# Kernel optimization log

Hardware: AMD Instinct MI355X
Metric: run time of the kernel (lower is better)

Reference implementation:

```python
import jax, jax.numpy as jnp
import numpy as np

N = 50000      # nodes
E = 800000     # edges
XS = 64        # x_size
ES = 32        # edge_attr dim (in_size = XS + ES = 96)
OUT = 64       # out_size
H = 128        # hidden_size
EPS = 1e-5


def _lin_init(k, fan_in, fan_out):
    s = 1.0 / np.sqrt(fan_in)
    kw, kb = jax.random.split(k)
    w = jax.random.uniform(kw, (fan_in, fan_out), minval=-s, maxval=s, dtype=jnp.float32)
    b = jax.random.uniform(kb, (fan_out,), minval=-s, maxval=s, dtype=jnp.float32)
    return w, b


def setup_inputs() -> dict:
    key = jax.random.key(0)
    ks = jax.random.split(key, 12)
    x = jax.random.normal(ks[0], (N, XS), dtype=jnp.float32)
    edge_index = jax.random.randint(ks[1], (2, E), 0, N, dtype=jnp.int64)
    edge_attr = jax.random.normal(ks[2], (E, ES), dtype=jnp.float32)
    u = jax.random.normal(ks[3], (1, 8), dtype=jnp.float32)
    batch = jnp.zeros((N,), dtype=jnp.int64)
    # MLP1: (96->128) LReLU (128->128) LReLU (128->64) LReLU LN(64)
    m1w0, m1b0 = _lin_init(ks[4], XS + ES, H)
    m1w1, m1b1 = _lin_init(ks[5], H, H)
    m1w2, m1b2 = _lin_init(ks[6], H, OUT)
    ln1_g = jnp.ones((OUT,), jnp.float32); ln1_b = jnp.zeros((OUT,), jnp.float32)
    # MLP2: (128->128) LReLU (128->128) LReLU (128->64) LReLU LN(64)
    m2w0, m2b0 = _lin_init(ks[7], XS + OUT, H)
    m2w1, m2b1 = _lin_init(ks[8], H, H)
    m2w2, m2b2 = _lin_init(ks[9], H, OUT)
    ln2_g = jnp.ones((OUT,), jnp.float32); ln2_b = jnp.zeros((OUT,), jnp.float32)
    return dict(x=x, edge_index=edge_index, edge_attr=edge_attr, u=u, batch=batch,
                m1w0=m1w0, m1b0=m1b0, m1w1=m1w1, m1b1=m1b1, m1w2=m1w2, m1b2=m1b2,
                ln1_g=ln1_g, ln1_b=ln1_b,
                m2w0=m2w0, m2b0=m2b0, m2w1=m2w1, m2b1=m2b1, m2w2=m2w2, m2b2=m2b2,
                ln2_g=ln2_g, ln2_b=ln2_b)


def _lrelu(v):
    return jax.nn.leaky_relu(v, 0.01)


def _layernorm(v, g, b):
    mu = jnp.mean(v, axis=-1, keepdims=True)
    var = jnp.mean(jnp.square(v - mu), axis=-1, keepdims=True)
    return (v - mu) * jax.lax.rsqrt(var + EPS) * g + b


def _mlp(h, w0, b0, w1, b1, w2, b2, g, bn):
    h = _lrelu(h @ w0 + b0)
    h = _lrelu(h @ w1 + b1)
    h = _lrelu(h @ w2 + b2)          # activate_last=True
    return _layernorm(h, g, bn)      # layer_norm=True


def reference(x, edge_index, edge_attr, u, batch,
              m1w0, m1b0, m1w1, m1b1, m1w2, m1b2, ln1_g, ln1_b,
              m2w0, m2b0, m2w1, m2b1, m2w2, m2b2, ln2_g, ln2_b):
    row, col = edge_index[0], edge_index[1]
    # gather source nodes, concat edge features -> per-edge MLP
    h = jnp.concatenate([x[row], edge_attr], axis=1)            # [E, 96]
    h = _mlp(h, m1w0, m1b0, m1w1, m1b1, m1w2, m1b2, ln1_g, ln1_b)  # [E, 64]
    # scatter_mean over destination nodes
    agg = jax.ops.segment_sum(h, col, num_segments=N)           # [N, 64]
    cnt = jax.ops.segment_sum(jnp.ones((E,), h.dtype), col, num_segments=N)
    agg = agg / jnp.maximum(cnt, 1.0)[:, None]
    # node update MLP
    h2 = jnp.concatenate([x, agg], axis=1)                      # [N, 128]
    return _mlp(h2, m2w0, m2b0, m2w1, m2b1, m2w2, m2b2, ln2_g, ln2_b)
```

## Files before the change

### kernel.cpp

```cpp
#include <hip/hip_runtime.h>


#define NNODES 50000
#define NEDGES 800000
#define NTILES_E2 3125
#define NTILES_N2 196

typedef __bf16 bf16;
typedef __bf16 __attribute__((ext_vector_type(4))) bf16x4;
typedef __bf16 __attribute__((ext_vector_type(8))) bf16x8;
typedef float __attribute__((ext_vector_type(4))) f32x4;

__device__ __forceinline__ f32x4 mfma_bf16(bf16x8 a, bf16x8 b, f32x4 c) {
    return __builtin_amdgcn_mfma_f32_16x16x32_bf16(a, b, c, 0, 0, 0);
}

__global__ void prep_weights(const float* __restrict__ w10, const float* __restrict__ w11,
                             const float* __restrict__ w12, const float* __restrict__ w20,
                             const float* __restrict__ w21, const float* __restrict__ w22,
                             bf16* __restrict__ img) {
    int idx = blockIdx.x * 256 + threadIdx.x;
    float f;
    if (idx < 13312) {
        int n = idx / 104, k = idx % 104;
        f = (k < 96) ? w10[k * 128 + n] : 0.0f;
    } else if (idx < 30720) {
        int t = idx - 13312; int n = t / 136, k = t % 136;
        f = (k < 128) ? w11[k * 128 + n] : 0.0f;
    } else if (idx < 39424) {
        int t = idx - 30720; int n = t / 136, k = t % 136;
        f = (k < 128) ? w12[k * 64 + n] : 0.0f;
    } else if (idx < 56832) {
        int t = idx - 39424; int n = t / 136, k = t % 136;
        f = (k < 128) ? w20[k * 128 + n] : 0.0f;
    } else if (idx < 74240) {
        int t = idx - 56832; int n = t / 136, k = t % 136;
        f = (k < 128) ? w21[k * 128 + n] : 0.0f;
    } else if (idx < 82944) {
        int t = idx - 74240; int n = t / 136, k = t % 136;
        f = (k < 128) ? w22[k * 64 + n] : 0.0f;
    } else {
        return;
    }
    img[idx] = (bf16)f;
}

__global__ void hist_kernel(const int* __restrict__ col, int* __restrict__ hist) {
    int i = blockIdx.x * 512 + threadIdx.x;
    if (i < NEDGES) {
        int d = col[i];
        if ((unsigned)d < (unsigned)NNODES) atomicAdd(hist + d, 1);
    }
}

__global__ void scanA(const int* __restrict__ hist, int* __restrict__ off,
                      int* __restrict__ csum) {
    __shared__ int sd[512];
    int t = threadIdx.x, i = blockIdx.x * 512 + t;
    int v = (i < NNODES) ? hist[i] : 0;
    sd[t] = v;
    __syncthreads();
    for (int o2 = 1; o2 < 512; o2 <<= 1) {
        int x = (t >= o2) ? sd[t - o2] : 0;
        __syncthreads();
        sd[t] += x;
        __syncthreads();
    }
    if (i < NNODES) off[i] = sd[t] - v;
    if (t == 511) csum[blockIdx.x] = sd[511];
}

__global__ void scanB(int* __restrict__ csum) {
    __shared__ int sd[128];
    int t = threadIdx.x;
    int v = (t < 98) ? csum[t] : 0;
    sd[t] = v;
    __syncthreads();
    for (int o2 = 1; o2 < 128; o2 <<= 1) {
        int x = (t >= o2) ? sd[t - o2] : 0;
        __syncthreads();
        sd[t] += x;
        __syncthreads();
    }
    if (t < 98) csum[t] = sd[t] - v;
}

__global__ void scanC(int* __restrict__ off, const int* __restrict__ csum) {
    int i = blockIdx.x * 512 + threadIdx.x;
    if (i < NNODES) off[i] += csum[blockIdx.x];
}

__global__ void scatter_kernel(const int* __restrict__ eidx, int* __restrict__ off,
                               int* __restrict__ perm, int* __restrict__ rdS) {
    int i = blockIdx.x * 512 + threadIdx.x;
    if (i < NEDGES) {
        int r = eidx[i], d = eidx[NEDGES + i];
        if ((unsigned)d < (unsigned)NNODES && (unsigned)r < (unsigned)NNODES) {
            int pos = atomicAdd(off + d, 1);
            if ((unsigned)pos < (unsigned)NEDGES) {
                perm[pos] = i;
                rdS[pos] = (int)(((unsigned)r & 0xFFFFu) | ((unsigned)d << 16));
            }
        }
    }
}

__global__ __launch_bounds__(512, 2) void edge_mlp(
    const float* __restrict__ x, const int* __restrict__ perm,
    const int* __restrict__ rdS, const float* __restrict__ eattr,
    const bf16* __restrict__ wimg,
    const float* __restrict__ b0g, const float* __restrict__ b1g,
    const float* __restrict__ b2g, const float* __restrict__ lng,
    const float* __restrict__ lnb, float* __restrict__ agg) {
    __shared__ __align__(16) bf16 wall[39424];
    __shared__ __align__(16) bf16 buf[256 * 136];
    __shared__ float bs[448];
    __shared__ int dstile[256];

    const int tid = threadIdx.x;
    {
        const uint4* src = (const uint4*)wimg;
        uint4* dst = (uint4*)wall;
        for (int i = tid; i < 4928; i += 512) dst[i] = src[i];
    }
    if (tid < 128) { bs[tid] = b0g[tid]; bs[128 + tid] = b1g[tid]; }
    else if (tid < 192) {
        int t = tid - 128;
        bs[256 + t] = b2g[t]; bs[320 + t] = lng[t]; bs[384 + t] = lnb[t];
    }
    __syncthreads();

    const int lane = tid & 63;
    const int wv = tid >> 6;
    const int col16 = lane & 15;
    const int quad = lane >> 4;

    float b0r[8], b1r[8], b2r[4], gr[4], br[4];
#pragma unroll
    for (int i = 0; i < 8; i++) { b0r[i] = bs[i * 16 + col16]; b1r[i] = bs[128 + i * 16 + col16]; }
#pragma unroll
    for (int i = 0; i < 4; i++) {
        b2r[i] = bs[256 + i * 16 + col16];
        gr[i] = bs[320 + i * 16 + col16];
        br[i] = bs[384 + i * 16 + col16];
    }

    const bf16* w0t = wall;
    const bf16* w1t = wall + 13312;
    const bf16* w2t = wall + 30720;

    const f32x4 vzero = {0.0f, 0.0f, 0.0f, 0.0f};
    const int r0 = wv * 32 + col16;
    const int rw = wv * 32 + quad * 4;
    const int el = tid >> 1, half = tid & 1;
    const int G = gridDim.x;

    int tile = blockIdx.x;

    float4 xr[8], er[4];
    unsigned cv;
    {
        int s = tile * 256 + el;
        cv = (unsigned)rdS[s];
        int ce = perm[s];
        int r = (int)(cv & 0xFFFFu); if (r >= NNODES) r = 0;
        if ((unsigned)ce >= (unsigned)NEDGES) ce = 0;
        const float4* xs = (const float4*)(x + (size_t)r * 64) + half * 8;
        const float4* es = (const float4*)(eattr + (size_t)ce * 32) + half * 4;
#pragma unroll
        for (int j = 0; j < 8; j++) xr[j] = xs[j];
#pragma unroll
        for (int j = 0; j < 4; j++) er[j] = es[j];
    }
    unsigned nv; int ne;
    {
        int t1 = tile + G;
        int s = (t1 < NTILES_E2 ? t1 * 256 : 0) + el;
        nv = (unsigned)rdS[s];
        ne = perm[s];
    }

    for (; tile < NTILES_E2; tile += G) {
        {
            unsigned d = cv >> 16;
            if (half == 0) dstile[el] = (d < (unsigned)NNODES) ? (int)d : 0;
            bf16* arow = buf + el * 136;
#pragma unroll
            for (int j = 0; j < 8; j++) {
                float4 vv = xr[j];
                bf16x4 u = {(bf16)vv.x, (bf16)vv.y, (bf16)vv.z, (bf16)vv.w};
                *(bf16x4*)(arow + half * 32 + j * 4) = u;
            }
#pragma unroll
            for (int j = 0; j < 4; j++) {
                float4 vv = er[j];
                bf16x4 u = {(bf16)vv.x, (bf16)vv.y, (bf16)vv.z, (bf16)vv.w};
                *(bf16x4*)(arow + 64 + half * 16 + j * 4) = u;
            }
        }
        __syncthreads();

        {
            int t2 = tile + G;
            if (t2 < NTILES_E2) {
                int r = (int)(nv & 0xFFFFu); if (r >= NNODES) r = 0;
                int e = ne; if ((unsigned)e >= (unsigned)NEDGES) e = 0;
                const float4* xs = (const float4*)(x + (size_t)r * 64) + half * 8;
                const float4* es = (const float4*)(eattr + (size_t)e * 32) + half * 4;
#pragma unroll
                for (int j = 0; j < 8; j++) xr[j] = xs[j];
#pragma unroll
                for (int j = 0; j < 4; j++) er[j] = es[j];
            }
        }
        unsigned pv; int pe;
        {
            int t3 = tile + 2 * G;
            int s = (t3 < NTILES_E2 ? t3 * 256 : 0) + el;
            pv = (unsigned)rdS[s];
            pe = perm[s];
        }

        f32x4 acc1[2][8];
#pragma unroll
        for (int mt = 0; mt < 2; mt++)
#pragma unroll
            for (int nt = 0; nt < 8; nt++) acc1[mt][nt] = vzero;
#pragma unroll
        for (int ks = 0; ks < 3; ks++) {
            bf16x8 a0 = *(const bf16x8*)(buf + r0 * 136 + ks * 32 + quad * 8);
            bf16x8 a1 = *(const bf16x8*)(buf + (r0 + 16) * 136 + ks * 32 + quad * 8);
#pragma unroll
            for (int nt = 0; nt < 8; nt++) {
                bf16x8 b = *(const bf16x8*)(w0t + (nt * 16 + col16) * 104 + ks * 32 + quad * 8);
                acc1[0][nt] = mfma_bf16(a0, b, acc1[0][nt]);
                acc1[1][nt] = mfma_bf16(a1, b, acc1[1][nt]);
            }
        }
#pragma unroll
        for (int mt = 0; mt < 2; mt++)
#pragma unroll
            for (int nt = 0; nt < 8; nt++)
#pragma unroll
                for (int rg = 0; rg < 4; rg++) {
                    float v = acc1[mt][nt][rg] + b0r[nt];
                    v = (v > 0.0f) ? v : 0.01f * v;
                    buf[(rw + mt * 16 + rg) * 136 + nt * 16 + col16] = (bf16)v;
                }

        bf16x8 a2[2][4];
#pragma unroll
        for (int mt = 0; mt < 2; mt++)
#pragma unroll
            for (int ks = 0; ks < 4; ks++)
                a2[mt][ks] = *(const bf16x8*)(buf + (r0 + mt * 16) * 136 + ks * 32 + quad * 8);
        f32x4 acc2[2][8];
#pragma unroll
        for (int mt = 0; mt < 2; mt++)
#pragma unroll
            for (int nt = 0; nt < 8; nt++) acc2[mt][nt] = vzero;
#pragma unroll
        for (int ks = 0; ks < 4; ks++) {
#pragma unroll
            for (int nt = 0; nt < 8; nt++) {
                bf16x8 b = *(const bf16x8*)(w1t + (nt * 16 + col16) * 136 + ks * 32 + quad * 8);
                acc2[0][nt] = mfma_bf16(a2[0][ks], b, acc2[0][nt]);
                acc2[1][nt] = mfma_bf16(a2[1][ks], b, acc2[1][nt]);
            }
        }
#pragma unroll
        for (int mt = 0; mt < 2; mt++)
#pragma unroll
            for (int nt = 0; nt < 8; nt++)
#pragma unroll
                for (int rg = 0; rg < 4; rg++) {
                    float v = acc2[mt][nt][rg] + b1r[nt];
                    v = (v > 0.0f) ? v : 0.01f * v;
                    buf[(rw + mt * 16 + rg) * 136 + nt * 16 + col16] = (bf16)v;
                }

        bf16x8 a3[2][4];
#pragma unroll
        for (int mt = 0; mt < 2; mt++)
#pragma unroll
            for (int ks = 0; ks < 4; ks++)
                a3[mt][ks] = *(const bf16x8*)(buf + (r0 + mt * 16) * 136 + ks * 32 + quad * 8);
        f32x4 acc3[2][4];
#pragma unroll
        for (int mt = 0; mt < 2; mt++)
#pragma unroll
            for (int nt = 0; nt < 4; nt++) acc3[mt][nt] = vzero;
#pragma unroll
        for (int ks = 0; ks < 4; ks++) {
#pragma unroll
            for (int nt = 0; nt < 4; nt++) {
                bf16x8 b = *(const bf16x8*)(w2t + (nt * 16 + col16) * 136 + ks * 32 + quad * 8);
                acc3[0][nt] = mfma_bf16(a3[0][ks], b, acc3[0][nt]);
                acc3[1][nt] = mfma_bf16(a3[1][ks], b, acc3[1][nt]);
            }
        }

        int drA[2][4];
#pragma unroll
        for (int mt = 0; mt < 2; mt++)
#pragma unroll
            for (int rg = 0; rg < 4; rg++) {
                int c = dstile[rw + mt * 16 + rg];
                drA[mt][rg] = ((unsigned)c < (unsigned)NNODES) ? c : 0;
            }
        __syncthreads();

#pragma unroll
        for (int mt = 0; mt < 2; mt++) {
            float vals[4][4];
            float s1[4] = {0.f, 0.f, 0.f, 0.f}, s2[4] = {0.f, 0.f, 0.f, 0.f};
#pragma unroll
            for (int nt = 0; nt < 4; nt++)
#pragma unroll
                for (int rg = 0; rg < 4; rg++) {
                    float v = acc3[mt][nt][rg] + b2r[nt];
                    v = (v > 0.0f) ? v : 0.01f * v;
                    vals[nt][rg] = v;
                    s1[rg] += v;
                    s2[rg] += v * v;
                }
#pragma unroll
            for (int off2 = 1; off2 < 16; off2 <<= 1) {
#pragma unroll
                for (int rg = 0; rg < 4; rg++) {
                    s1[rg] += __shfl_xor(s1[rg], off2);
                    s2[rg] += __shfl_xor(s2[rg], off2);
                }
            }
            float o[4][4];
#pragma unroll
            for (int rg = 0; rg < 4; rg++) {
                float mu = s1[rg] * 0.015625f;
                float var = s2[rg] * 0.015625f - mu * mu;
                float rstd = rsqrtf(var + 1e-5f);
#pragma unroll
                for (int nt = 0; nt < 4; nt++)
                    o[nt][rg] = (vals[nt][rg] - mu) * rstd * gr[nt] + br[nt];
            }
            float run0 = o[0][0], run1 = o[1][0], run2 = o[2][0], run3 = o[3][0];
            int cur = drA[mt][0];
#pragma unroll
            for (int rg = 1; rg < 4; rg++) {
                if (drA[mt][rg] != cur) {
                    float* dst = agg + (size_t)cur * 64 + col16;
                    atomicAdd(dst, run0); atomicAdd(dst + 16, run1);
                    atomicAdd(dst + 32, run2); atomicAdd(dst + 48, run3);
                    run0 = o[0][rg]; run1 = o[1][rg]; run2 = o[2][rg]; run3 = o[3][rg];
                    cur = drA[mt][rg];
                } else {
                    run0 += o[0][rg]; run1 += o[1][rg]; run2 += o[2][rg]; run3 += o[3][rg];
                }
            }
            float* dst = agg + (size_t)cur * 64 + col16;
            atomicAdd(dst, run0); atomicAdd(dst + 16, run1);
            atomicAdd(dst + 32, run2); atomicAdd(dst + 48, run3);
        }

        cv = nv; nv = pv; ne = pe;
    }
}

__global__ __launch_bounds__(512, 2) void node_mlp(
    const float* __restrict__ x, const float* __restrict__ agg,
    const int* __restrict__ hist, const bf16* __restrict__ wimg,
    const float* __restrict__ b0g, const float* __restrict__ b1g,
    const float* __restrict__ b2g, const float* __restrict__ lng,
    const float* __restrict__ lnb, float* __restrict__ out) {
    __shared__ __align__(16) bf16 wall[43520];
    __shared__ __align__(16) bf16 buf[256 * 136];
    __shared__ float bs[448];

    const int tid = threadIdx.x;
    {
        const uint4* src = (const uint4*)wimg;
        uint4* dst = (uint4*)wall;
        for (int i = tid; i < 5440; i += 512) dst[i] = src[i];
    }
    if (tid < 128) { bs[tid] = b0g[tid]; bs[128 + tid] = b1g[tid]; }
    else if (tid < 192) {
        int t = tid - 128;
        bs[256 + t] = b2g[t]; bs[320 + t] = lng[t]; bs[384 + t] = lnb[t];
    }
    __syncthreads();

    const int lane = tid & 63;
    const int wv = tid >> 6;
    const int col16 = lane & 15;
    const int quad = lane >> 4;

    float b0r[8], b1r[8], b2r[4], gr[4], br[4];
#pragma unroll
    for (int i = 0; i < 8; i++) { b0r[i] = bs[i * 16 + col16]; b1r[i] = bs[128 + i * 16 + col16]; }
#pragma unroll
    for (int i = 0; i < 4; i++) {
        b2r[i] = bs[256 + i * 16 + col16];
        gr[i] = bs[320 + i * 16 + col16];
        br[i] = bs[384 + i * 16 + col16];
    }

    const bf16* w0t = wall;
    const bf16* w1t = wall + 17408;
    const bf16* w2t = wall + 34816;

    const f32x4 vzero = {0.0f, 0.0f, 0.0f, 0.0f};
    const int r0 = wv * 32 + col16;
    const int rw = wv * 32 + quad * 4;
    const int el = tid >> 1, half = tid & 1;
    const int G = gridDim.x;

    int tile = blockIdx.x;
    if (tile >= NTILES_N2) return;

    float4 xr[8], ar[8];
    int cc;
    {
        int i = tile * 256 + el;
        if (i >= NNODES) i = NNODES - 1;
        const float4* xs = (const float4*)(x + (size_t)i * 64) + half * 8;
        const float4* as = (const float4*)(agg + (size_t)i * 64) + half * 8;
#pragma unroll
        for (int j = 0; j < 8; j++) { xr[j] = xs[j]; ar[j] = as[j]; }
        cc = hist[i];
    }

    for (; tile < NTILES_N2; tile += G) {
        const int nbase = tile * 256;
        {
            float inv = 1.0f / (float)(cc > 1 ? cc : 1);
            bf16* arow = buf + el * 136;
#pragma unroll
            for (int j = 0; j < 8; j++) {
                float4 v = xr[j];
                bf16x4 u = {(bf16)v.x, (bf16)v.y, (bf16)v.z, (bf16)v.w};
                *(bf16x4*)(arow + half * 32 + j * 4) = u;
            }
#pragma unroll
            for (int j = 0; j < 8; j++) {
                float4 v = ar[j];
                bf16x4 u = {(bf16)(v.x * inv), (bf16)(v.y * inv), (bf16)(v.z * inv), (bf16)(v.w * inv)};
                *(bf16x4*)(arow + 64 + half * 32 + j * 4) = u;
            }
        }
        __syncthreads();

        {
            int t2 = tile + G;
            if (t2 < NTILES_N2) {
                int i = t2 * 256 + el;
                if (i >= NNODES) i = NNODES - 1;
                const float4* xs = (const float4*)(x + (size_t)i * 64) + half * 8;
                const float4* as = (const float4*)(agg + (size_t)i * 64) + half * 8;
#pragma unroll
                for (int j = 0; j < 8; j++) { xr[j] = xs[j]; ar[j] = as[j]; }
                cc = hist[i];
            }
        }

        f32x4 acc1[2][8];
#pragma unroll
        for (int mt = 0; mt < 2; mt++)
#pragma unroll
            for (int nt = 0; nt < 8; nt++) acc1[mt][nt] = vzero;
#pragma unroll
        for (int ks = 0; ks < 4; ks++) {
            bf16x8 a0 = *(const bf16x8*)(buf + r0 * 136 + ks * 32 + quad * 8);
            bf16x8 a1 = *(const bf16x8*)(buf + (r0 + 16) * 136 + ks * 32 + quad * 8);
#pragma unroll
            for (int nt = 0; nt < 8; nt++) {
                bf16x8 b = *(const bf16x8*)(w0t + (nt * 16 + col16) * 136 + ks * 32 + quad * 8);
                acc1[0][nt] = mfma_bf16(a0, b, acc1[0][nt]);
                acc1[1][nt] = mfma_bf16(a1, b, acc1[1][nt]);
            }
        }
#pragma unroll
        for (int mt = 0; mt < 2; mt++)
#pragma unroll
            for (int nt = 0; nt < 8; nt++)
#pragma unroll
                for (int rg = 0; rg < 4; rg++) {
                    float v = acc1[mt][nt][rg] + b0r[nt];
                    v = (v > 0.0f) ? v : 0.01f * v;
                    buf[(rw + mt * 16 + rg) * 136 + nt * 16 + col16] = (bf16)v;
                }

        bf16x8 a2[2][4];
#pragma unroll
        for (int mt = 0; mt < 2; mt++)
#pragma unroll
            for (int ks = 0; ks < 4; ks++)
                a2[mt][ks] = *(const bf16x8*)(buf + (r0 + mt * 16) * 136 + ks * 32 + quad * 8);
        f32x4 acc2[2][8];
#pragma unroll
        for (int mt = 0; mt < 2; mt++)
#pragma unroll
            for (int nt = 0; nt < 8; nt++) acc2[mt][nt] = vzero;
#pragma unroll
        for (int ks = 0; ks < 4; ks++) {
#pragma unroll
            for (int nt = 0; nt < 8; nt++) {
                bf16x8 b = *(const bf16x8*)(w1t + (nt * 16 + col16) * 136 + ks * 32 + quad * 8);
                acc2[0][nt] = mfma_bf16(a2[0][ks], b, acc2[0][nt]);
                acc2[1][nt] = mfma_bf16(a2[1][ks], b, acc2[1][nt]);
            }
        }
#pragma unroll
        for (int mt = 0; mt < 2; mt++)
#pragma unroll
            for (int nt = 0; nt < 8; nt++)
#pragma unroll
                for (int rg = 0; rg < 4; rg++) {
                    float v = acc2[mt][nt][rg] + b1r[nt];
                    v = (v > 0.0f) ? v : 0.01f * v;
                    buf[(rw + mt * 16 + rg) * 136 + nt * 16 + col16] = (bf16)v;
                }

        bf16x8 a3[2][4];
#pragma unroll
        for (int mt = 0; mt < 2; mt++)
#pragma unroll
            for (int ks = 0; ks < 4; ks++)
                a3[mt][ks] = *(const bf16x8*)(buf + (r0 + mt * 16) * 136 + ks * 32 + quad * 8);
        f32x4 acc3[2][4];
#pragma unroll
        for (int mt = 0; mt < 2; mt++)
#pragma unroll
            for (int nt = 0; nt < 4; nt++) acc3[mt][nt] = vzero;
#pragma unroll
        for (int ks = 0; ks < 4; ks++) {
#pragma unroll
            for (int nt = 0; nt < 4; nt++) {
                bf16x8 b = *(const bf16x8*)(w2t + (nt * 16 + col16) * 136 + ks * 32 + quad * 8);
                acc3[0][nt] = mfma_bf16(a3[0][ks], b, acc3[0][nt]);
                acc3[1][nt] = mfma_bf16(a3[1][ks], b, acc3[1][nt]);
            }
        }
        __syncthreads();

#pragma unroll
        for (int mt = 0; mt < 2; mt++) {
            float vals[4][4];
            float s1[4] = {0.f, 0.f, 0.f, 0.f}, s2[4] = {0.f, 0.f, 0.f, 0.f};
#pragma unroll
            for (int nt = 0; nt < 4; nt++)
#pragma unroll
                for (int rg = 0; rg < 4; rg++) {
                    float v = acc3[mt][nt][rg] + b2r[nt];
                    v = (v > 0.0f) ? v : 0.01f * v;
                    vals[nt][rg] = v;
                    s1[rg] += v;
                    s2[rg] += v * v;
                }
#pragma unroll
            for (int off2 = 1; off2 < 16; off2 <<= 1) {
#pragma unroll
                for (int rg = 0; rg < 4; rg++) {
                    s1[rg] += __shfl_xor(s1[rg], off2);
                    s2[rg] += __shfl_xor(s2[rg], off2);
                }
            }
#pragma unroll
            for (int rg = 0; rg < 4; rg++) {
                float mu = s1[rg] * 0.015625f;
                float var = s2[rg] * 0.015625f - mu * mu;
                float rstd = rsqrtf(var + 1e-5f);
                int i = nbase + rw + mt * 16 + rg;
                if (i < NNODES) {
#pragma unroll
                    for (int nt = 0; nt < 4; nt++) {
                        float o = (vals[nt][rg] - mu) * rstd * gr[nt] + br[nt];
                        out[(size_t)i * 64 + nt * 16 + col16] = o;
                    }
                }
            }
        }
    }
}

extern "C" void kernel_launch(void* const* d_in, const int* in_sizes, int n_in,
                              void* d_out, int out_size, void* d_ws, size_t ws_size,
                              hipStream_t stream) {
    (void)in_sizes; (void)n_in; (void)out_size; (void)ws_size;
    const float* x     = (const float*)d_in[0];
    const int*   eidx  = (const int*)d_in[1];
    const float* eattr = (const float*)d_in[2];
    const float* m1w0 = (const float*)d_in[5];
    const float* m1b0 = (const float*)d_in[6];
    const float* m1w1 = (const float*)d_in[7];
    const float* m1b1 = (const float*)d_in[8];
    const float* m1w2 = (const float*)d_in[9];
    const float* m1b2 = (const float*)d_in[10];
    const float* ln1g = (const float*)d_in[11];
    const float* ln1b = (const float*)d_in[12];
    const float* m2w0 = (const float*)d_in[13];
    const float* m2b0 = (const float*)d_in[14];
    const float* m2w1 = (const float*)d_in[15];
    const float* m2b1 = (const float*)d_in[16];
    const float* m2w2 = (const float*)d_in[17];
    const float* m2b2 = (const float*)d_in[18];
    const float* ln2g = (const float*)d_in[19];
    const float* ln2b = (const float*)d_in[20];

    char* ws = (char*)d_ws;
    float* agg  = (float*)ws;
    int*   hist = (int*)(ws + 12800000);
    int*   off  = (int*)(ws + 13000000);
    int*   csum = (int*)(ws + 13200000);
    int*   perm = (int*)(ws + 13200512);
    int*   rdS  = (int*)(ws + 16400512);
    bf16*  wimg = (bf16*)(ws + 19600512);

    hipMemsetAsync(d_ws, 0, 13000000, stream);
    prep_weights<<<324, 256, 0, stream>>>(m1w0, m1w1, m1w2, m2w0, m2w1, m2w2, wimg);
    hist_kernel<<<1563, 512, 0, stream>>>(eidx + NEDGES, hist);
    scanA<<<98, 512, 0, stream>>>(hist, off, csum);
    scanB<<<1, 128, 0, stream>>>(csum);
    scanC<<<98, 512, 0, stream>>>(off, csum);
    scatter_kernel<<<1563, 512, 0, stream>>>(eidx, off, perm, rdS);
    edge_mlp<<<256, 512, 0, stream>>>(x, perm, rdS, eattr, wimg, m1b0, m1b1, m1b2,
                                      ln1g, ln1b, agg);
    node_mlp<<<196, 512, 0, stream>>>(x, agg, hist, wimg + 39424,
                                      m2b0, m2b1, m2b2, ln2g, ln2b, (float*)d_out);
}
```

Baseline: 489.6 us.

## Double block size to 1024 threads with one 16-row tile per wave

Both MLP kernels now run 1024-thread blocks. Each wave handles a single 16-row M tile instead of two, and four threads load each row instead of two. This halves accumulator and prefetch register pressure and puts more waves on each CU to hide gather latency. The node kernel also drops its persistent loop and prefetch, processing one tile per block. In exchange each wave reuses each loaded weight fragment for half as many MFMAs, so LDS traffic per MFMA rises.

```diff
diff --git a/kernel.cpp b/kernel.cpp
--- a/kernel.cpp
+++ b/kernel.cpp
@@ -105,7 +105,7 @@
     }
 }
 
-__global__ __launch_bounds__(512, 2) void edge_mlp(
+__global__ __launch_bounds__(1024) void edge_mlp(
     const float* __restrict__ x, const int* __restrict__ perm,
     const int* __restrict__ rdS, const float* __restrict__ eattr,
     const bf16* __restrict__ wimg,
@@ -121,7 +121,7 @@
     {
         const uint4* src = (const uint4*)wimg;
         uint4* dst = (uint4*)wall;
-        for (int i = tid; i < 4928; i += 512) dst[i] = src[i];
+        for (int i = tid; i < 4928; i += 1024) dst[i] = src[i];
     }
     if (tid < 128) { bs[tid] = b0g[tid]; bs[128 + tid] = b1g[tid]; }
     else if (tid < 192) {
@@ -150,14 +150,14 @@
     const bf16* w2t = wall + 30720;
 
     const f32x4 vzero = {0.0f, 0.0f, 0.0f, 0.0f};
-    const int r0 = wv * 32 + col16;
-    const int rw = wv * 32 + quad * 4;
-    const int el = tid >> 1, half = tid & 1;
+    const int r0 = wv * 16 + col16;
+    const int rw = wv * 16 + quad * 4;
+    const int el = tid >> 2, part = tid & 3;
     const int G = gridDim.x;
 
     int tile = blockIdx.x;
 
-    float4 xr[8], er[4];
+    float4 xr[4], er[2];
     unsigned cv;
     {
         int s = tile * 256 + el;
@@ -165,12 +165,12 @@
         int ce = perm[s];
         int r = (int)(cv & 0xFFFFu); if (r >= NNODES) r = 0;
         if ((unsigned)ce >= (unsigned)NEDGES) ce = 0;
-        const float4* xs = (const float4*)(x + (size_t)r * 64) + half * 8;
-        const float4* es = (const float4*)(eattr + (size_t)ce * 32) + half * 4;
-#pragma unroll
-        for (int j = 0; j < 8; j++) xr[j] = xs[j];
-#pragma unroll
-        for (int j = 0; j < 4; j++) er[j] = es[j];
+        const float4* xs = (const float4*)(x + (size_t)r * 64) + part * 4;
+        const float4* es = (const float4*)(eattr + (size_t)ce * 32) + part * 2;
+#pragma unroll
+        for (int j = 0; j < 4; j++) xr[j] = xs[j];
+#pragma unroll
+        for (int j = 0; j < 2; j++) er[j] = es[j];
     }
     unsigned nv; int ne;
     {
@@ -183,19 +183,19 @@
     for (; tile < NTILES_E2; tile += G) {
         {
             unsigned d = cv >> 16;
-            if (half == 0) dstile[el] = (d < (unsigned)NNODES) ? (int)d : 0;
+            if (part == 0) dstile[el] = (d < (unsigned)NNODES) ? (int)d : 0;
             bf16* arow = buf + el * 136;
 #pragma unroll
-            for (int j = 0; j < 8; j++) {
+            for (int j = 0; j < 4; j++) {
                 float4 vv = xr[j];
                 bf16x4 u = {(bf16)vv.x, (bf16)vv.y, (bf16)vv.z, (bf16)vv.w};
-                *(bf16x4*)(arow + half * 32 + j * 4) = u;
-            }
-#pragma unroll
-            for (int j = 0; j < 4; j++) {
+                *(bf16x4*)(arow + part * 16 + j * 4) = u;
+            }
+#pragma unroll
+            for (int j = 0; j < 2; j++) {
                 float4 vv = er[j];
                 bf16x4 u = {(bf16)vv.x, (bf16)vv.y, (bf16)vv.z, (bf16)vv.w};
-                *(bf16x4*)(arow + 64 + half * 16 + j * 4) = u;
+                *(bf16x4*)(arow + 64 + part * 8 + j * 4) = u;
             }
         }
         __syncthreads();
@@ -205,12 +205,12 @@
             if (t2 < NTILES_E2) {
                 int r = (int)(nv & 0xFFFFu); if (r >= NNODES) r = 0;
                 int e = ne; if ((unsigned)e >= (unsigned)NEDGES) e = 0;
-                const float4* xs = (const float4*)(x + (size_t)r * 64) + half * 8;
-                const float4* es = (const float4*)(eattr + (size_t)e * 32) + half * 4;
-#pragma unroll
-                for (int j = 0; j < 8; j++) xr[j] = xs[j];
-#pragma unroll
-                for (int j = 0; j < 4; j++) er[j] = es[j];
+                const float4* xs = (const float4*)(x + (size_t)r * 64) + part * 4;
+                const float4* es = (const float4*)(eattr + (size_t)e * 32) + part * 2;
+#pragma unroll
+                for (int j = 0; j < 4; j++) xr[j] = xs[j];
+#pragma unroll
+                for (int j = 0; j < 2; j++) er[j] = es[j];
             }
         }
         unsigned pv; int pe;
@@ -221,104 +221,83 @@
             pe = perm[s];
         }
 
-        f32x4 acc1[2][8];
-#pragma unroll
-        for (int mt = 0; mt < 2; mt++)
-#pragma unroll
-            for (int nt = 0; nt < 8; nt++) acc1[mt][nt] = vzero;
+        f32x4 acc1[8];
+#pragma unroll
+        for (int nt = 0; nt < 8; nt++) acc1[nt] = vzero;
 #pragma unroll
         for (int ks = 0; ks < 3; ks++) {
             bf16x8 a0 = *(const bf16x8*)(buf + r0 * 136 + ks * 32 + quad * 8);
-            bf16x8 a1 = *(const bf16x8*)(buf + (r0 + 16) * 136 + ks * 32 + quad * 8);
 #pragma unroll
             for (int nt = 0; nt < 8; nt++) {
                 bf16x8 b = *(const bf16x8*)(w0t + (nt * 16 + col16) * 104 + ks * 32 + quad * 8);
-                acc1[0][nt] = mfma_bf16(a0, b, acc1[0][nt]);
-                acc1[1][nt] = mfma_bf16(a1, b, acc1[1][nt]);
-            }
-        }
-#pragma unroll
-        for (int mt = 0; mt < 2; mt++)
-#pragma unroll
-            for (int nt = 0; nt < 8; nt++)
-#pragma unroll
-                for (int rg = 0; rg < 4; rg++) {
-                    float v = acc1[mt][nt][rg] + b0r[nt];
-                    v = (v > 0.0f) ? v : 0.01f * v;
-                    buf[(rw + mt * 16 + rg) * 136 + nt * 16 + col16] = (bf16)v;
-                }
-
-        bf16x8 a2[2][4];
-#pragma unroll
-        for (int mt = 0; mt < 2; mt++)
-#pragma unroll
-            for (int ks = 0; ks < 4; ks++)
-                a2[mt][ks] = *(const bf16x8*)(buf + (r0 + mt * 16) * 136 + ks * 32 + quad * 8);
-        f32x4 acc2[2][8];
-#pragma unroll
-        for (int mt = 0; mt < 2; mt++)
-#pragma unroll
-            for (int nt = 0; nt < 8; nt++) acc2[mt][nt] = vzero;
+                acc1[nt] = mfma_bf16(a0, b, acc1[nt]);
+            }
+        }
+#pragma unroll
+        for (int nt = 0; nt < 8; nt++)
+#pragma unroll
+            for (int rg = 0; rg < 4; rg++) {
+                float v = acc1[nt][rg] + b0r[nt];
+                v = (v > 0.0f) ? v : 0.01f * v;
+                buf[(rw + rg) * 136 + nt * 16 + col16] = (bf16)v;
+            }
+
+        bf16x8 a2[4];
+#pragma unroll
+        for (int ks = 0; ks < 4; ks++)
+            a2[ks] = *(const bf16x8*)(buf + r0 * 136 + ks * 32 + quad * 8);
+        f32x4 acc2[8];
+#pragma unroll
+        for (int nt = 0; nt < 8; nt++) acc2[nt] = vzero;
 #pragma unroll
         for (int ks = 0; ks < 4; ks++) {
 #pragma unroll
             for (int nt = 0; nt < 8; nt++) {
                 bf16x8 b = *(const bf16x8*)(w1t + (nt * 16 + col16) * 136 + ks * 32 + quad * 8);
-                acc2[0][nt] = mfma_bf16(a2[0][ks], b, acc2[0][nt]);
-                acc2[1][nt] = mfma_bf16(a2[1][ks], b, acc2[1][nt]);
-            }
-        }
-#pragma unroll
-        for (int mt = 0; mt < 2; mt++)
-#pragma unroll
-            for (int nt = 0; nt < 8; nt++)
-#pragma unroll
-                for (int rg = 0; rg < 4; rg++) {
-                    float v = acc2[mt][nt][rg] + b1r[nt];
-                    v = (v > 0.0f) ? v : 0.01f * v;
-                    buf[(rw + mt * 16 + rg) * 136 + nt * 16 + col16] = (bf16)v;
-                }
-
-        bf16x8 a3[2][4];
-#pragma unroll
-        for (int mt = 0; mt < 2; mt++)
-#pragma unroll
-            for (int ks = 0; ks < 4; ks++)
-                a3[mt][ks] = *(const bf16x8*)(buf + (r0 + mt * 16) * 136 + ks * 32 + quad * 8);
-        f32x4 acc3[2][4];
-#pragma unroll
-        for (int mt = 0; mt < 2; mt++)
-#pragma unroll
-            for (int nt = 0; nt < 4; nt++) acc3[mt][nt] = vzero;
+                acc2[nt] = mfma_bf16(a2[ks], b, acc2[nt]);
+            }
+        }
+#pragma unroll
+        for (int nt = 0; nt < 8; nt++)
+#pragma unroll
+            for (int rg = 0; rg < 4; rg++) {
+                float v = acc2[nt][rg] + b1r[nt];
+                v = (v > 0.0f) ? v : 0.01f * v;
+                buf[(rw + rg) * 136 + nt * 16 + col16] = (bf16)v;
+            }
+
+        bf16x8 a3[4];
+#pragma unroll
+        for (int ks = 0; ks < 4; ks++)
+            a3[ks] = *(const bf16x8*)(buf + r0 * 136 + ks * 32 + quad * 8);
+        f32x4 acc3[4];
+#pragma unroll
+        for (int nt = 0; nt < 4; nt++) acc3[nt] = vzero;
 #pragma unroll
         for (int ks = 0; ks < 4; ks++) {
 #pragma unroll
             for (int nt = 0; nt < 4; nt++) {
                 bf16x8 b = *(const bf16x8*)(w2t + (nt * 16 + col16) * 136 + ks * 32 + quad * 8);
-                acc3[0][nt] = mfma_bf16(a3[0][ks], b, acc3[0][nt]);
-                acc3[1][nt] = mfma_bf16(a3[1][ks], b, acc3[1][nt]);
-            }
-        }
-
-        int drA[2][4];
-#pragma unroll
-        for (int mt = 0; mt < 2; mt++)
-#pragma unroll
-            for (int rg = 0; rg < 4; rg++) {
-                int c = dstile[rw + mt * 16 + rg];
-                drA[mt][rg] = ((unsigned)c < (unsigned)NNODES) ? c : 0;
-            }
+                acc3[nt] = mfma_bf16(a3[ks], b, acc3[nt]);
+            }
+        }
+
+        int drA[4];
+#pragma unroll
+        for (int rg = 0; rg < 4; rg++) {
+            int c = dstile[rw + rg];
+            drA[rg] = ((unsigned)c < (unsigned)NNODES) ? c : 0;
+        }
         __syncthreads();
 
-#pragma unroll
-        for (int mt = 0; mt < 2; mt++) {
+        {
             float vals[4][4];
             float s1[4] = {0.f, 0.f, 0.f, 0.f}, s2[4] = {0.f, 0.f, 0.f, 0.f};
 #pragma unroll
             for (int nt = 0; nt < 4; nt++)
 #pragma unroll
                 for (int rg = 0; rg < 4; rg++) {
-                    float v = acc3[mt][nt][rg] + b2r[nt];
+                    float v = acc3[nt][rg] + b2r[nt];
                     v = (v > 0.0f) ? v : 0.01f * v;
                     vals[nt][rg] = v;
                     s1[rg] += v;
@@ -343,15 +322,15 @@
                     o[nt][rg] = (vals[nt][rg] - mu) * rstd * gr[nt] + br[nt];
             }
             float run0 = o[0][0], run1 = o[1][0], run2 = o[2][0], run3 = o[3][0];
-            int cur = drA[mt][0];
+            int cur = drA[0];
 #pragma unroll
             for (int rg = 1; rg < 4; rg++) {
-                if (drA[mt][rg] != cur) {
+                if (drA[rg] != cur) {
                     float* dst = agg + (size_t)cur * 64 + col16;
                     atomicAdd(dst, run0); atomicAdd(dst + 16, run1);
                     atomicAdd(dst + 32, run2); atomicAdd(dst + 48, run3);
                     run0 = o[0][rg]; run1 = o[1][rg]; run2 = o[2][rg]; run3 = o[3][rg];
-                    cur = drA[mt][rg];
+                    cur = drA[rg];
                 } else {
                     run0 += o[0][rg]; run1 += o[1][rg]; run2 += o[2][rg]; run3 += o[3][rg];
                 }
@@ -365,7 +344,7 @@
     }
 }
 
-__global__ __launch_bounds__(512, 2) void node_mlp(
+__global__ __launch_bounds__(1024) void node_mlp(
     const float* __restrict__ x, const float* __restrict__ agg,
     const int* __restrict__ hist, const bf16* __restrict__ wimg,
     const float* __restrict__ b0g, const float* __restrict__ b1g,
@@ -379,19 +358,43 @@
     {
         const uint4* src = (const uint4*)wimg;
         uint4* dst = (uint4*)wall;
-        for (int i = tid; i < 5440; i += 512) dst[i] = src[i];
+        for (int i = tid; i < 5440; i += 1024) dst[i] = src[i];
     }
     if (tid < 128) { bs[tid] = b0g[tid]; bs[128 + tid] = b1g[tid]; }
     else if (tid < 192) {
         int t = tid - 128;
         bs[256 + t] = b2g[t]; bs[320 + t] = lng[t]; bs[384 + t] = lnb[t];
     }
-    __syncthreads();
 
     const int lane = tid & 63;
     const int wv = tid >> 6;
     const int col16 = lane & 15;
     const int quad = lane >> 4;
+    const int el = tid >> 2, part = tid & 3;
+
+    const int nbase = blockIdx.x * 256;
+    {
+        int i = nbase + el;
+        if (i >= NNODES) i = NNODES - 1;
+        const float4* xs = (const float4*)(x + (size_t)i * 64) + part * 4;
+        const float4* as = (const float4*)(agg + (size_t)i * 64) + part * 4;
+        int c = hist[i];
+        float inv = 1.0f / (float)(c > 1 ? c : 1);
+        bf16* arow = buf + el * 136;
+#pragma unroll
+        for (int j = 0; j < 4; j++) {
+            float4 v = xs[j];
+            bf16x4 u = {(bf16)v.x, (bf16)v.y, (bf16)v.z, (bf16)v.w};
+            *(bf16x4*)(arow + part * 16 + j * 4) = u;
+        }
+#pragma unroll
+        for (int j = 0; j < 4; j++) {
+            float4 v = as[j];
+            bf16x4 u = {(bf16)(v.x * inv), (bf16)(v.y * inv), (bf16)(v.z * inv), (bf16)(v.w * inv)};
+            *(bf16x4*)(arow + 64 + part * 16 + j * 4) = u;
+        }
+    }
+    __syncthreads();
 
     float b0r[8], b1r[8], b2r[4], gr[4], br[4];
 #pragma unroll
@@ -408,173 +411,102 @@
     const bf16* w2t = wall + 34816;
 
     const f32x4 vzero = {0.0f, 0.0f, 0.0f, 0.0f};
-    const int r0 = wv * 32 + col16;
-    const int rw = wv * 32 + quad * 4;
-    const int el = tid >> 1, half = tid & 1;
-    const int G = gridDim.x;
-
-    int tile = blockIdx.x;
-    if (tile >= NTILES_N2) return;
-
-    float4 xr[8], ar[8];
-    int cc;
+    const int r0 = wv * 16 + col16;
+    const int rw = wv * 16 + quad * 4;
+
+    f32x4 acc1[8];
+#pragma unroll
+    for (int nt = 0; nt < 8; nt++) acc1[nt] = vzero;
+#pragma unroll
+    for (int ks = 0; ks < 4; ks++) {
+        bf16x8 a0 = *(const bf16x8*)(buf + r0 * 136 + ks * 32 + quad * 8);
+#pragma unroll
+        for (int nt = 0; nt < 8; nt++) {
+            bf16x8 b = *(const bf16x8*)(w0t + (nt * 16 + col16) * 136 + ks * 32 + quad * 8);
+            acc1[nt] = mfma_bf16(a0, b, acc1[nt]);
+        }
+    }
+#pragma unroll
+    for (int nt = 0; nt < 8; nt++)
+#pragma unroll
+        for (int rg = 0; rg < 4; rg++) {
+            float v = acc1[nt][rg] + b0r[nt];
+            v = (v > 0.0f) ? v : 0.01f * v;
+            buf[(rw + rg) * 136 + nt * 16 + col16] = (bf16)v;
+        }
+
+    bf16x8 a2[4];
+#pragma unroll
+    for (int ks = 0; ks < 4; ks++)
+        a2[ks] = *(const bf16x8*)(buf + r0 * 136 + ks * 32 + quad * 8);
+    f32x4 acc2[8];
+#pragma unroll
+    for (int nt = 0; nt < 8; nt++) acc2[nt] = vzero;
+#pragma unroll
+    for (int ks = 0; ks < 4; ks++) {
+#pragma unroll
+        for (int nt = 0; nt < 8; nt++) {
+            bf16x8 b = *(const bf16x8*)(w1t + (nt * 16 + col16) * 136 + ks * 32 + quad * 8);
+            acc2[nt] = mfma_bf16(a2[ks], b, acc2[nt]);
+        }
+    }
+#pragma unroll
+    for (int nt = 0; nt < 8; nt++)
+#pragma unroll
+        for (int rg = 0; rg < 4; rg++) {
+            float v = acc2[nt][rg] + b1r[nt];
+            v = (v > 0.0f) ? v : 0.01f * v;
+            buf[(rw + rg) * 136 + nt * 16 + col16] = (bf16)v;
+        }
+
+    bf16x8 a3[4];
+#pragma unroll
+    for (int ks = 0; ks < 4; ks++)
+        a3[ks] = *(const bf16x8*)(buf + r0 * 136 + ks * 32 + quad * 8);
+    f32x4 acc3[4];
+#pragma unroll
+    for (int nt = 0; nt < 4; nt++) acc3[nt] = vzero;
+#pragma unroll
+    for (int ks = 0; ks < 4; ks++) {
+#pragma unroll
+        for (int nt = 0; nt < 4; nt++) {
+            bf16x8 b = *(const bf16x8*)(w2t + (nt * 16 + col16) * 136 + ks * 32 + quad * 8);
+            acc3[nt] = mfma_bf16(a3[ks], b, acc3[nt]);
+        }
+    }
+
     {
-        int i = tile * 256 + el;
-        if (i >= NNODES) i = NNODES - 1;
-        const float4* xs = (const float4*)(x + (size_t)i * 64) + half * 8;
-        const float4* as = (const float4*)(agg + (size_t)i * 64) + half * 8;
-#pragma unroll
-        for (int j = 0; j < 8; j++) { xr[j] = xs[j]; ar[j] = as[j]; }
-        cc = hist[i];
-    }
-
-    for (; tile < NTILES_N2; tile += G) {
-        const int nbase = tile * 256;
-        {
-            float inv = 1.0f / (float)(cc > 1 ? cc : 1);
-            bf16* arow = buf + el * 136;
-#pragma unroll
-            for (int j = 0; j < 8; j++) {
-                float4 v = xr[j];
-                bf16x4 u = {(bf16)v.x, (bf16)v.y, (bf16)v.z, (bf16)v.w};
-                *(bf16x4*)(arow + half * 32 + j * 4) = u;
-            }
-#pragma unroll
-            for (int j = 0; j < 8; j++) {
-                float4 v = ar[j];
-                bf16x4 u = {(bf16)(v.x * inv), (bf16)(v.y * inv), (bf16)(v.z * inv), (bf16)(v.w * inv)};
-                *(bf16x4*)(arow + 64 + half * 32 + j * 4) = u;
-            }
-        }
-        __syncthreads();
-
-        {
-            int t2 = tile + G;
-            if (t2 < NTILES_N2) {
-                int i = t2 * 256 + el;
-                if (i >= NNODES) i = NNODES - 1;
-                const float4* xs = (const float4*)(x + (size_t)i * 64) + half * 8;
-                const float4* as = (const float4*)(agg + (size_t)i * 64) + half * 8;
-#pragma unroll
-                for (int j = 0; j < 8; j++) { xr[j] = xs[j]; ar[j] = as[j]; }
-                cc = hist[i];
-            }
-        }
-
-        f32x4 acc1[2][8];
-#pragma unroll
-        for (int mt = 0; mt < 2; mt++)
-#pragma unroll
-            for (int nt = 0; nt < 8; nt++) acc1[mt][nt] = vzero;
-#pragma unroll
-        for (int ks = 0; ks < 4; ks++) {
-            bf16x8 a0 = *(const bf16x8*)(buf + r0 * 136 + ks * 32 + quad * 8);
-            bf16x8 a1 = *(const bf16x8*)(buf + (r0 + 16) * 136 + ks * 32 + quad * 8);
-#pragma unroll
-            for (int nt = 0; nt < 8; nt++) {
-                bf16x8 b = *(const bf16x8*)(w0t + (nt * 16 + col16) * 136 + ks * 32 + quad * 8);
-                acc1[0][nt] = mfma_bf16(a0, b, acc1[0][nt]);
-                acc1[1][nt] = mfma_bf16(a1, b, acc1[1][nt]);
-            }
-        }
-#pragma unroll
-        for (int mt = 0; mt < 2; mt++)
-#pragma unroll
-            for (int nt = 0; nt < 8; nt++)
-#pragma unroll
-                for (int rg = 0; rg < 4; rg++) {
-                    float v = acc1[mt][nt][rg] + b0r[nt];
-                    v = (v > 0.0f) ? v : 0.01f * v;
-                    buf[(rw + mt * 16 + rg) * 136 + nt * 16 + col16] = (bf16)v;
-                }
-
-        bf16x8 a2[2][4];
-#pragma unroll
-        for (int mt = 0; mt < 2; mt++)
-#pragma unroll
-            for (int ks = 0; ks < 4; ks++)
-                a2[mt][ks] = *(const bf16x8*)(buf + (r0 + mt * 16) * 136 + ks * 32 + quad * 8);
-        f32x4 acc2[2][8];
-#pragma unroll
-        for (int mt = 0; mt < 2; mt++)
-#pragma unroll
-            for (int nt = 0; nt < 8; nt++) acc2[mt][nt] = vzero;
-#pragma unroll
-        for (int ks = 0; ks < 4; ks++) {
-#pragma unroll
-            for (int nt = 0; nt < 8; nt++) {
-                bf16x8 b = *(const bf16x8*)(w1t + (nt * 16 + col16) * 136 + ks * 32 + quad * 8);
-                acc2[0][nt] = mfma_bf16(a2[0][ks], b, acc2[0][nt]);
-                acc2[1][nt] = mfma_bf16(a2[1][ks], b, acc2[1][nt]);
-            }
-        }
-#pragma unroll
-        for (int mt = 0; mt < 2; mt++)
-#pragma unroll
-            for (int nt = 0; nt < 8; nt++)
-#pragma unroll
-                for (int rg = 0; rg < 4; rg++) {
-                    float v = acc2[mt][nt][rg] + b1r[nt];
-                    v = (v > 0.0f) ? v : 0.01f * v;
-                    buf[(rw + mt * 16 + rg) * 136 + nt * 16 + col16] = (bf16)v;
-                }
-
-        bf16x8 a3[2][4];
-#pragma unroll
-        for (int mt = 0; mt < 2; mt++)
-#pragma unroll
-            for (int ks = 0; ks < 4; ks++)
-                a3[mt][ks] = *(const bf16x8*)(buf + (r0 + mt * 16) * 136 + ks * 32 + quad * 8);
-        f32x4 acc3[2][4];
-#pragma unroll
-        for (int mt = 0; mt < 2; mt++)
-#pragma unroll
-            for (int nt = 0; nt < 4; nt++) acc3[mt][nt] = vzero;
-#pragma unroll
-        for (int ks = 0; ks < 4; ks++) {
-#pragma unroll
-            for (int nt = 0; nt < 4; nt++) {
-                bf16x8 b = *(const bf16x8*)(w2t + (nt * 16 + col16) * 136 + ks * 32 + quad * 8);
-                acc3[0][nt] = mfma_bf16(a3[0][ks], b, acc3[0][nt]);
-                acc3[1][nt] = mfma_bf16(a3[1][ks], b, acc3[1][nt]);
-            }
-        }
-        __syncthreads();
-
-#pragma unroll
-        for (int mt = 0; mt < 2; mt++) {
-            float vals[4][4];
-            float s1[4] = {0.f, 0.f, 0.f, 0.f}, s2[4] = {0.f, 0.f, 0.f, 0.f};
-#pragma unroll
-            for (int nt = 0; nt < 4; nt++)
-#pragma unroll
-                for (int rg = 0; rg < 4; rg++) {
-                    float v = acc3[mt][nt][rg] + b2r[nt];
-                    v = (v > 0.0f) ? v : 0.01f * v;
-                    vals[nt][rg] = v;
-                    s1[rg] += v;
-                    s2[rg] += v * v;
-                }
-#pragma unroll
-            for (int off2 = 1; off2 < 16; off2 <<= 1) {
-#pragma unroll
-                for (int rg = 0; rg < 4; rg++) {
-                    s1[rg] += __shfl_xor(s1[rg], off2);
-                    s2[rg] += __shfl_xor(s2[rg], off2);
-                }
-            }
+        float vals[4][4];
+        float s1[4] = {0.f, 0.f, 0.f, 0.f}, s2[4] = {0.f, 0.f, 0.f, 0.f};
+#pragma unroll
+        for (int nt = 0; nt < 4; nt++)
 #pragma unroll
             for (int rg = 0; rg < 4; rg++) {
-                float mu = s1[rg] * 0.015625f;
-                float var = s2[rg] * 0.015625f - mu * mu;
-                float rstd = rsqrtf(var + 1e-5f);
-                int i = nbase + rw + mt * 16 + rg;
-                if (i < NNODES) {
-#pragma unroll
-                    for (int nt = 0; nt < 4; nt++) {
-                        float o = (vals[nt][rg] - mu) * rstd * gr[nt] + br[nt];
-                        out[(size_t)i * 64 + nt * 16 + col16] = o;
-                    }
+                float v = acc3[nt][rg] + b2r[nt];
+                v = (v > 0.0f) ? v : 0.01f * v;
+                vals[nt][rg] = v;
+                s1[rg] += v;
+                s2[rg] += v * v;
+            }
+#pragma unroll
+        for (int off2 = 1; off2 < 16; off2 <<= 1) {
+#pragma unroll
+            for (int rg = 0; rg < 4; rg++) {
+                s1[rg] += __shfl_xor(s1[rg], off2);
+                s2[rg] += __shfl_xor(s2[rg], off2);
+            }
+        }
+#pragma unroll
+        for (int rg = 0; rg < 4; rg++) {
+            float mu = s1[rg] * 0.015625f;
+            float var = s2[rg] * 0.015625f - mu * mu;
+            float rstd = rsqrtf(var + 1e-5f);
+            int i = nbase + rw + rg;
+            if (i < NNODES) {
+#pragma unroll
+                for (int nt = 0; nt < 4; nt++) {
+                    float o = (vals[nt][rg] - mu) * rstd * gr[nt] + br[nt];
+                    out[(size_t)i * 64 + nt * 16 + col16] = o;
                 }
             }
         }
@@ -621,8 +553,8 @@
     scanB<<<1, 128, 0, stream>>>(csum);
     scanC<<<98, 512, 0, stream>>>(off, csum);
     scatter_kernel<<<1563, 512, 0, stream>>>(eidx, off, perm, rdS);
-    edge_mlp<<<256, 512, 0, stream>>>(x, perm, rdS, eattr, wimg, m1b0, m1b1, m1b2,
-                                      ln1g, ln1b, agg);
-    node_mlp<<<196, 512, 0, stream>>>(x, agg, hist, wimg + 39424,
-                                      m2b0, m2b1, m2b2, ln2g, ln2b, (float*)d_out);
-}
+    edge_mlp<<<256, 1024, 0, stream>>>(x, perm, rdS, eattr, wimg, m1b0, m1b1, m1b2,
+                                       ln1g, ln1b, agg);
+    node_mlp<<<196, 1024, 0, stream>>>(x, agg, hist, wimg + 39424,
+                                       m2b0, m2b1, m2b2, ln2g, ln2b, (float*)d_out);
+}
```

Result: slower. 509.9 us (+4.2%).
